# Optimization experiments

Hardware: AMD Instinct MI355X
Metric: run time of the kernel (lower is better)

## Reference

```python
import jax, jax.numpy as jnp
import numpy as np

H = 512   # encoding_size
T = 512   # sequence_length
B = 128   # batch


def setup_inputs() -> dict:
    key = jax.random.key(0)
    ks = jax.random.split(key, 12)
    s = 1.0 / np.sqrt(H)  # PyTorch default uniform init bound

    def u(k, shape):
        return jax.random.uniform(k, shape, jnp.float32, -s, s)

    return {
        "x": jax.random.normal(ks[0], (B, T), jnp.float32),
        "enc_Wi": u(ks[1], (3 * H, 1)),
        "enc_Wh": u(ks[2], (3 * H, H)),
        "enc_bi": u(ks[3], (3 * H,)),
        "enc_bh": u(ks[4], (3 * H,)),
        "dec_Wi": u(ks[5], (3 * H, 1)),
        "dec_Wh": u(ks[6], (3 * H, H)),
        "dec_bi": u(ks[7], (3 * H,)),
        "dec_bh": u(ks[8], (3 * H,)),
        "lin_W": u(ks[9], (1, H)),
        "lin_b": u(ks[10], (1,)),
    }


def gru_step(h, x, Wi, Wh, bi, bh):
    # PyTorch GRU cell: gates ordered [r, z, n]
    gx = x @ Wi.T + bi          # (B, 3H)
    gh = h @ Wh.T + bh          # (B, 3H)
    r = jax.nn.sigmoid(gx[:, :H] + gh[:, :H])
    z = jax.nn.sigmoid(gx[:, H:2 * H] + gh[:, H:2 * H])
    n = jnp.tanh(gx[:, 2 * H:] + r * gh[:, 2 * H:])
    return (1.0 - z) * n + z * h


def reference(x, enc_Wi, enc_Wh, enc_bi, enc_bh,
              dec_Wi, dec_Wh, dec_bi, dec_bh, lin_W, lin_b):
    x = x[:, :T]
    xs = x.T[:, :, None]  # (T, B, 1)
    h0 = jnp.zeros((x.shape[0], H), x.dtype)

    # Encoder GRU over the sequence
    def enc_body(h, xt):
        return gru_step(h, xt, enc_Wi, enc_Wh, enc_bi, enc_bh), None

    h, _ = jax.lax.scan(enc_body, h0, xs)

    y = h @ lin_W.T + lin_b  # (B, 1) initial decoder input

    def dec_body(carry, _):
        h, y = carry
        h = gru_step(h, y, dec_Wi, dec_Wh, dec_bi, dec_bh)
        y = h @ lin_W.T + lin_b
        return (h, y), y[:, 0]

    _, ys = jax.lax.scan(dec_body, (h, y), None, length=T)  # (T, B)

    return jnp.flip(ys.T, axis=1)  # (B, T), reversed in time
```

## Files before the change

### kernel.cpp

```cpp
#include <hip/hip_runtime.h>
#include <math.h>

#define HD 512
#define TT 512
#define NB 128
#define NBLK 512
#define NGRP 16
#define GBLK 32
#define NU 16
#define NBB 8
#define NTHR 512
#define HBUF_N (NB * HD)
#define SLOTP 64

typedef float v2f __attribute__((ext_vector_type(2)));
typedef float v4f __attribute__((ext_vector_type(4)));

__global__ void init_sync(int* s) {
    for (int i = threadIdx.x + blockIdx.x * 1024; i < NGRP * GBLK * SLOTP; i += 32768)
        s[i] = 0;
}

__device__ __forceinline__ float sigm(float v) { return 1.0f / (1.0f + __expf(-v)); }

__device__ __forceinline__ v2f pkfma(v2f a, v2f b, v2f c) {
    v2f d;
    asm("v_pk_fma_f32 %0, %1, %2, %3" : "=v"(d) : "v"(a), "v"(b), "v"(c));
    return d;
}
__device__ __forceinline__ v2f pkmul(v2f a, v2f b) {
    v2f d;
    asm("v_pk_mul_f32 %0, %1, %2" : "=v"(d) : "v"(a), "v"(b));
    return d;
}
__device__ __forceinline__ v2f vlo(v4f v) { return __builtin_shufflevector(v, v, 0, 1); }
__device__ __forceinline__ v2f vhi(v4f v) { return __builtin_shufflevector(v, v, 2, 3); }

#define H_LOAD(p)    __hip_atomic_load((p), __ATOMIC_RELAXED, __HIP_MEMORY_SCOPE_AGENT)
#define H_STORE(p,v) __hip_atomic_store((p), (v), __ATOMIC_RELAXED, __HIP_MEMORY_SCOPE_AGENT)

#define MERGE(A, B, bit)                                                        \
    ((((kq & (bit)) ? (B) : (A))) +                                             \
     __shfl_xor(((kq & (bit)) ? (A) : (B)), (bit)))

#define STAGE(PAR)                                                              \
  { const float* srcp = hbuf + (PAR) * HBUF_N + (size_t)b0 * HD;                \
    float vv[NBB];                                                              \
    _Pragma("unroll") for (int i = 0; i < NBB; ++i)                             \
      vv[i] = H_LOAD(srcp + i * HD + tid);                                      \
    _Pragma("unroll") for (int i = 0; i < NBB; ++i) hs[i][tid] = vv[i]; }

#define GBAR()                                                                  \
  { __syncthreads();                                                            \
    ++phase;                                                                    \
    if (tid == 0) H_STORE(myflag, phase);                                       \
    if (tid < GBLK) {                                                           \
      const int* sl = gflags + tid * SLOTP;                                     \
      while (H_LOAD(sl) < phase) __builtin_amdgcn_s_sleep(2);                   \
    }                                                                           \
    __syncthreads(); }

#define STEP(XV, WBUF)                                                          \
  { float a_[3][NBB];                                                           \
    _Pragma("unroll") for (int b = 0; b < NBB; ++b) {                           \
      v4f hb0 = *(const v4f*)&hs[b][4 * kq];                                    \
      v4f hb1 = *(const v4f*)&hs[b][4 * kq + 128];                              \
      v4f hb2 = *(const v4f*)&hs[b][4 * kq + 256];                              \
      v4f hb3 = *(const v4f*)&hs[b][4 * kq + 384];                              \
      _Pragma("unroll") for (int g = 0; g < 3; ++g) {                           \
        v2f t = pkmul(wW2[g][0], vlo(hb0));                                     \
        t = pkfma(wW2[g][1], vhi(hb0), t);                                      \
        t = pkfma(wW2[g][2], vlo(hb1), t);                                      \
        t = pkfma(wW2[g][3], vhi(hb1), t);                                      \
        t = pkfma(wW2[g][4], vlo(hb2), t);                                      \
        t = pkfma(wW2[g][5], vhi(hb2), t);                                      \
        t = pkfma(wW2[g][6], vlo(hb3), t);                                      \
        t = pkfma(wW2[g][7], vhi(hb3), t);                                      \
        a_[g][b] = t.x + t.y;                                                   \
      } }                                                                       \
    float r_[3];                                                                \
    _Pragma("unroll") for (int g = 0; g < 3; ++g) {                             \
      const float m0 = MERGE(a_[g][0], a_[g][1], 1);                            \
      const float m1 = MERGE(a_[g][2], a_[g][3], 1);                            \
      const float m2 = MERGE(a_[g][4], a_[g][5], 1);                            \
      const float m3 = MERGE(a_[g][6], a_[g][7], 1);                            \
      const float n0 = MERGE(m0, m1, 2);                                        \
      const float n1 = MERGE(m2, m3, 2);                                        \
      float q = MERGE(n0, n1, 4);                                               \
      q += __shfl_xor(q, 8);                                                    \
      q += __shfl_xor(q, 16);                                                   \
      r_[g] = q;                                                                \
    }                                                                           \
    if (kq < NBB) {                                                             \
      const float xv = (XV);                                                    \
      const float r = sigm(fmaf(xv, wi_r, c_r) + r_[0]);                        \
      const float z = sigm(fmaf(xv, wi_z, c_z) + r_[1]);                        \
      const float n = tanhf(fmaf(xv, wi_n, bi_n) + r * (r_[2] + bh_n));         \
      const float hp = hs[kq][ur];                                              \
      H_STORE((WBUF) + (size_t)(b0 + kq) * HD + ur, fmaf(z, hp - n, n));        \
    } }

__global__ __launch_bounds__(NTHR, 2) void gru_persist(
    const float* __restrict__ x,
    const float* __restrict__ eWi, const float* __restrict__ eWh,
    const float* __restrict__ ebi, const float* __restrict__ ebh,
    const float* __restrict__ dWi, const float* __restrict__ dWh,
    const float* __restrict__ dbi, const float* __restrict__ dbh,
    const float* __restrict__ linW, const float* __restrict__ linb,
    float* __restrict__ hbuf, int* __restrict__ sync_w,
    float* __restrict__ out)
{
    const int blk = blockIdx.x;
    const int g   = blk >> 5;
    const int us  = blk & 31;
    const int b0  = g * NBB;
    const int u0  = us * NU;
    const int tid = threadIdx.x;
    const int u   = tid >> 5;
    const int kq  = tid & 31;
    const int ur  = u0 + u;

    __shared__ float hs[NBB][HD];
    __shared__ float xs[NBB][HD];
    __shared__ float lin_s[HD];
    __shared__ float y_s[NBB];

    int* gflags = sync_w + g * GBLK * SLOTP;
    int* myflag = gflags + us * SLOTP;
    int  phase  = 0;

    v2f wW2[3][8];
    #pragma unroll
    for (int g3 = 0; g3 < 3; ++g3) {
        const size_t row = (size_t)(g3 * HD + ur) * HD;
        #pragma unroll
        for (int i = 0; i < 4; ++i) {
            const v4f w = *(const v4f*)&eWh[row + i * 128 + 4 * kq];
            wW2[g3][2 * i]     = vlo(w);
            wW2[g3][2 * i + 1] = vhi(w);
        }
    }
    float wi_r = eWi[ur], wi_z = eWi[HD + ur], wi_n = eWi[2 * HD + ur];
    float c_r  = ebi[ur] + ebh[ur];
    float c_z  = ebi[HD + ur] + ebh[HD + ur];
    float bi_n = ebi[2 * HD + ur], bh_n = ebh[2 * HD + ur];
    lin_s[tid] = linW[tid];
    const float lb = linb[0];
    #pragma unroll
    for (int i = 0; i < NBB; ++i)
        xs[i][tid] = x[(size_t)(b0 + i) * TT + tid];

    for (int s = 0; s < TT; ++s) {
        if (s == 0) {
            #pragma unroll
            for (int i = 0; i < NBB; ++i) hs[i][tid] = 0.f;
        } else {
            STAGE((s + 1) & 1);
        }
        __syncthreads();
        STEP(xs[kq][s], hbuf + (s & 1) * HBUF_N);
        GBAR();
    }

    #pragma unroll
    for (int g3 = 0; g3 < 3; ++g3) {
        const size_t row = (size_t)(g3 * HD + ur) * HD;
        #pragma unroll
        for (int i = 0; i < 4; ++i) {
            const v4f w = *(const v4f*)&dWh[row + i * 128 + 4 * kq];
            wW2[g3][2 * i]     = vlo(w);
            wW2[g3][2 * i + 1] = vhi(w);
        }
    }
    wi_r = dWi[ur]; wi_z = dWi[HD + ur]; wi_n = dWi[2 * HD + ur];
    c_r  = dbi[ur] + dbh[ur];
    c_z  = dbi[HD + ur] + dbh[HD + ur];
    bi_n = dbi[2 * HD + ur]; bh_n = dbh[2 * HD + ur];

    for (int s = 0; s <= TT; ++s) {
        STAGE((s + 1) & 1);
        __syncthreads();
        {
            const int b = tid >> 6, k64 = tid & 63;
            float p = 0.f;
            #pragma unroll
            for (int i = 0; i < 2; ++i) {
                const float4 hv = *(const float4*)&hs[b][4 * k64 + 256 * i];
                const float4 lv = *(const float4*)&lin_s[4 * k64 + 256 * i];
                p = fmaf(hv.x, lv.x, p); p = fmaf(hv.y, lv.y, p);
                p = fmaf(hv.z, lv.z, p); p = fmaf(hv.w, lv.w, p);
            }
            p += __shfl_xor(p, 1);  p += __shfl_xor(p, 2);  p += __shfl_xor(p, 4);
            p += __shfl_xor(p, 8);  p += __shfl_xor(p, 16); p += __shfl_xor(p, 32);
            if (k64 == 0) y_s[b] = p + lb;
        }
        __syncthreads();
        if (s >= 1 && us == 0 && tid < NBB)
            out[(size_t)(b0 + tid) * TT + (TT - s)] = y_s[tid];
        if (s < TT) {
            STEP(y_s[kq], hbuf + (s & 1) * HBUF_N);
            GBAR();
        }
    }
}

extern "C" void kernel_launch(void* const* d_in, const int* in_sizes, int n_in,
                              void* d_out, int out_size, void* d_ws, size_t ws_size,
                              hipStream_t stream) {
    const float* x    = (const float*)d_in[0];
    const float* eWi  = (const float*)d_in[1];
    const float* eWh  = (const float*)d_in[2];
    const float* ebi  = (const float*)d_in[3];
    const float* ebh  = (const float*)d_in[4];
    const float* dWi  = (const float*)d_in[5];
    const float* dWh  = (const float*)d_in[6];
    const float* dbi  = (const float*)d_in[7];
    const float* dbh  = (const float*)d_in[8];
    const float* linW = (const float*)d_in[9];
    const float* linb = (const float*)d_in[10];
    float* out  = (float*)d_out;

    float* hbuf   = (float*)d_ws;
    int*   sync_w = (int*)(hbuf + 2 * HBUF_N);

    init_sync<<<32, 1024, 0, stream>>>(sync_w);
    gru_persist<<<dim3(NBLK), dim3(NTHR), 0, stream>>>(
        x, eWi, eWh, ebi, ebh, dWi, dWh, dbi, dbh, linW, linb,
        hbuf, sync_w, out);
}
```

Baseline: 4.480 ms.

## Split group barrier into two halves to overlap matvec with remaining producers

```diff
diff --git a/kernel.cpp b/kernel.cpp
--- a/kernel.cpp
+++ b/kernel.cpp
@@ -43,42 +43,51 @@
     ((((kq & (bit)) ? (B) : (A))) +                                             \
      __shfl_xor(((kq & (bit)) ? (A) : (B)), (bit)))
 
-#define STAGE(PAR)                                                              \
-  { const float* srcp = hbuf + (PAR) * HBUF_N + (size_t)b0 * HD;                \
-    float vv[NBB];                                                              \
-    _Pragma("unroll") for (int i = 0; i < NBB; ++i)                             \
-      vv[i] = H_LOAD(srcp + i * HD + tid);                                      \
-    _Pragma("unroll") for (int i = 0; i < NBB; ++i) hs[i][tid] = vv[i]; }
-
-#define GBAR()                                                                  \
-  { __syncthreads();                                                            \
-    ++phase;                                                                    \
-    if (tid == 0) H_STORE(myflag, phase);                                       \
-    if (tid < GBLK) {                                                           \
-      const int* sl = gflags + tid * SLOTP;                                     \
+#define WAIT_HALF(BASE)                                                         \
+  { if (tid < 16) {                                                             \
+      const int* sl = gflags + ((BASE) + tid) * SLOTP;                          \
       while (H_LOAD(sl) < phase) __builtin_amdgcn_s_sleep(2);                   \
     }                                                                           \
     __syncthreads(); }
 
-#define STEP(XV, WBUF)                                                          \
-  { float a_[3][NBB];                                                           \
-    _Pragma("unroll") for (int b = 0; b < NBB; ++b) {                           \
-      v4f hb0 = *(const v4f*)&hs[b][4 * kq];                                    \
-      v4f hb1 = *(const v4f*)&hs[b][4 * kq + 128];                              \
-      v4f hb2 = *(const v4f*)&hs[b][4 * kq + 256];                              \
-      v4f hb3 = *(const v4f*)&hs[b][4 * kq + 384];                              \
-      _Pragma("unroll") for (int g = 0; g < 3; ++g) {                           \
-        v2f t = pkmul(wW2[g][0], vlo(hb0));                                     \
-        t = pkfma(wW2[g][1], vhi(hb0), t);                                      \
-        t = pkfma(wW2[g][2], vlo(hb1), t);                                      \
-        t = pkfma(wW2[g][3], vhi(hb1), t);                                      \
-        t = pkfma(wW2[g][4], vlo(hb2), t);                                      \
-        t = pkfma(wW2[g][5], vhi(hb2), t);                                      \
-        t = pkfma(wW2[g][6], vlo(hb3), t);                                      \
-        t = pkfma(wW2[g][7], vhi(hb3), t);                                      \
-        a_[g][b] = t.x + t.y;                                                   \
-      } }                                                                       \
-    float r_[3];                                                                \
+#define STAGE_H(PAR, HALF)                                                      \
+  { const float* srcp = hbuf + (PAR) * HBUF_N + (size_t)b0 * HD + (HALF) * 256; \
+    float vv[4];                                                                \
+    _Pragma("unroll") for (int i = 0; i < 4; ++i) {                             \
+      const int idx = i * NTHR + tid;                                           \
+      vv[i] = H_LOAD(srcp + (idx >> 8) * HD + (idx & 255));                     \
+    }                                                                           \
+    _Pragma("unroll") for (int i = 0; i < 4; ++i) {                             \
+      const int idx = i * NTHR + tid;                                           \
+      hs[idx >> 8][(HALF) * 256 + (idx & 255)] = vv[i];                         \
+    } }
+
+#define STEP_A                                                                  \
+  _Pragma("unroll") for (int b = 0; b < NBB; ++b) {                             \
+    v4f hb0 = *(const v4f*)&hs[b][4 * kq];                                      \
+    v4f hb1 = *(const v4f*)&hs[b][4 * kq + 128];                                \
+    _Pragma("unroll") for (int g = 0; g < 3; ++g) {                             \
+      v2f t = pkmul(wW2[g][0], vlo(hb0));                                       \
+      t = pkfma(wW2[g][1], vhi(hb0), t);                                        \
+      t = pkfma(wW2[g][2], vlo(hb1), t);                                        \
+      t = pkfma(wW2[g][3], vhi(hb1), t);                                        \
+      a_[g][b] = t.x + t.y;                                                     \
+    } }
+
+#define STEP_B                                                                  \
+  _Pragma("unroll") for (int b = 0; b < NBB; ++b) {                             \
+    v4f hb2 = *(const v4f*)&hs[b][4 * kq + 256];                                \
+    v4f hb3 = *(const v4f*)&hs[b][4 * kq + 384];                                \
+    _Pragma("unroll") for (int g = 0; g < 3; ++g) {                             \
+      v2f t = pkmul(wW2[g][4], vlo(hb2));                                       \
+      t = pkfma(wW2[g][5], vhi(hb2), t);                                        \
+      t = pkfma(wW2[g][6], vlo(hb3), t);                                        \
+      t = pkfma(wW2[g][7], vhi(hb3), t);                                        \
+      a_[g][b] += t.x + t.y;                                                    \
+    } }
+
+#define STEP_FIN(XV, WBUF)                                                      \
+  { float r_[3];                                                                \
     _Pragma("unroll") for (int g = 0; g < 3; ++g) {                             \
       const float m0 = MERGE(a_[g][0], a_[g][1], 1);                            \
       const float m1 = MERGE(a_[g][2], a_[g][3], 1);                            \
@@ -100,6 +109,11 @@
       H_STORE((WBUF) + (size_t)(b0 + kq) * HD + ur, fmaf(z, hp - n, n));        \
     } }
 
+#define FLAG_DONE()                                                             \
+  { __syncthreads();                                                            \
+    ++phase;                                                                    \
+    if (tid == 0) H_STORE(myflag, phase); }
+
 __global__ __launch_bounds__(NTHR, 2) void gru_persist(
     const float* __restrict__ x,
     const float* __restrict__ eWi, const float* __restrict__ eWh,
@@ -150,16 +164,29 @@
     for (int i = 0; i < NBB; ++i)
         xs[i][tid] = x[(size_t)(b0 + i) * TT + tid];
 
-    for (int s = 0; s < TT; ++s) {
-        if (s == 0) {
-            #pragma unroll
-            for (int i = 0; i < NBB; ++i) hs[i][tid] = 0.f;
-        } else {
-            STAGE((s + 1) & 1);
-        }
-        __syncthreads();
-        STEP(xs[kq][s], hbuf + (s & 1) * HBUF_N);
-        GBAR();
+    {
+        #pragma unroll
+        for (int i = 0; i < NBB; ++i) hs[i][tid] = 0.f;
+        __syncthreads();
+        float a_[3][NBB];
+        STEP_A;
+        STEP_B;
+        STEP_FIN(xs[kq][0], hbuf);
+        FLAG_DONE();
+    }
+
+    for (int s = 1; s < TT; ++s) {
+        float a_[3][NBB];
+        WAIT_HALF(0);
+        STAGE_H((s + 1) & 1, 0);
+        __syncthreads();
+        STEP_A;
+        WAIT_HALF(16);
+        STAGE_H((s + 1) & 1, 1);
+        __syncthreads();
+        STEP_B;
+        STEP_FIN(xs[kq][s], hbuf + (s & 1) * HBUF_N);
+        FLAG_DONE();
     }
 
     #pragma unroll
@@ -178,7 +205,13 @@
     bi_n = dbi[2 * HD + ur]; bh_n = dbh[2 * HD + ur];
 
     for (int s = 0; s <= TT; ++s) {
-        STAGE((s + 1) & 1);
+        float a_[3][NBB];
+        WAIT_HALF(0);
+        STAGE_H((s + 1) & 1, 0);
+        __syncthreads();
+        if (s < TT) { STEP_A; }
+        WAIT_HALF(16);
+        STAGE_H((s + 1) & 1, 1);
         __syncthreads();
         {
             const int b = tid >> 6, k64 = tid & 63;
@@ -194,12 +227,13 @@
             p += __shfl_xor(p, 8);  p += __shfl_xor(p, 16); p += __shfl_xor(p, 32);
             if (k64 == 0) y_s[b] = p + lb;
         }
+        if (s < TT) { STEP_B; }
         __syncthreads();
         if (s >= 1 && us == 0 && tid < NBB)
             out[(size_t)(b0 + tid) * TT + (TT - s)] = y_s[tid];
         if (s < TT) {
-            STEP(y_s[kq], hbuf + (s & 1) * HBUF_N);
-            GBAR();
+            STEP_FIN(y_s[kq], hbuf + (s & 1) * HBUF_N);
+            FLAG_DONE();
         }
     }
 }
```

Result: slower. 8.833 ms (+97.2%).
